# Optimization experiments

Hardware: AMD Instinct MI355X
Metric: run time of the kernel (lower is better)

Reference implementation:

```python
import jax, jax.numpy as jnp
import numpy as np

NUM_HEADS = 8
WIN = 3


def setup_inputs() -> dict:
    key = jax.random.key(0)
    ks = jax.random.split(key, 7)
    C = 64
    b, H, W = 8, 64, 64
    x = jax.random.normal(ks[0], (b, C, H, W), jnp.float32)
    W_qk = jax.random.normal(ks[1], (C, 2 * C), jnp.float32) * 0.05
    b_qk = jax.random.normal(ks[2], (2 * C,), jnp.float32) * 0.05
    W_kv = jax.random.normal(ks[3], (C, 2 * C), jnp.float32) * 0.05
    b_kv = jax.random.normal(ks[4], (2 * C,), jnp.float32) * 0.05
    W_proj = jax.random.normal(ks[5], (C, C), jnp.float32) * 0.05
    b_proj = jax.random.normal(ks[6], (C,), jnp.float32) * 0.05
    return {"x": x, "W_qk": W_qk, "b_qk": b_qk, "W_kv": W_kv, "b_kv": b_kv,
            "W_proj": W_proj, "b_proj": b_proj}


def reference(x, W_qk, b_qk, W_kv, b_kv, W_proj, b_proj):
    b, C, H, W = x.shape
    hd = C // NUM_HEADS
    scale = hd ** -0.5
    B = b * H * W
    L = WIN * WIN

    # Reflection pad (1,1,1,1) then extract all 3x3 windows (stride 1) -> one window per pixel.
    xp = jnp.pad(x, ((0, 0), (0, 0), (1, 1), (1, 1)), mode="reflect")  # (b,C,H+2,W+2)
    patches = jnp.stack(
        [xp[:, :, i:i + H, j:j + W] for i in range(WIN) for j in range(WIN)],
        axis=2,
    )  # (b, C, 9, H, W)
    patches = jnp.transpose(patches, (0, 3, 4, 1, 2))  # (b, H, W, C, 9)
    # Faithful to torch: contiguous (B, C, 3, 3).reshape(B, L, C) scrambles C and L.
    xs = patches.reshape(B, L, C)  # (B, 9, C) -- scrambled layout, as in original

    # pooling_size=1 -> AvgPool2d identity; g_pooling = mean over the 9 tokens
    x_g = jnp.mean(xs, axis=1, keepdims=True)            # (B, 1, C)
    x_f = jnp.concatenate([x_g, xs], axis=1)             # (B, 10, C)
    N = x_f.shape[1]

    # x_raw: per-pixel token, order (b h w) matches window order
    x_raw = jnp.transpose(x, (0, 2, 3, 1)).reshape(B, C)  # (B, C)

    # q / q_ projections
    qk = x_raw @ W_qk + b_qk                              # (B, 2C)
    q = qk[:, :C].reshape(B, NUM_HEADS, hd)               # (B, h, d)
    q_ = qk[:, C:].reshape(B, NUM_HEADS, hd)              # (B, h, d)
    q_value = jnp.sum(q * q_, axis=-1, keepdims=True)     # (B, h, 1)

    # k / v projections over pooled-global + window tokens
    kv = (x_f @ W_kv + b_kv).reshape(B, N, 2, NUM_HEADS, hd)
    k = jnp.transpose(kv[:, :, 0], (0, 2, 1, 3))          # (B, h, N, d)
    v = jnp.transpose(kv[:, :, 1], (0, 2, 1, 3))          # (B, h, N, d)

    logits = jnp.einsum("bhd,bhnd->bhn", q * scale, k)    # (B, h, N)
    logits = jnp.concatenate([logits, q_value], axis=-1)  # (B, h, N+1)
    attn = jax.nn.softmax(logits, axis=-1)

    x_fusion = jnp.einsum("bhn,bhnd->bhd", attn[..., :N], v)  # (B, h, d)
    x_sole = attn[..., N:] * q_                               # (B, h, d)
    out = (x_sole + x_fusion).reshape(B, C)                   # concat heads

    out = out @ W_proj + b_proj                               # (B, C)
    out = out.reshape(b, H, W, C).transpose(0, 3, 1, 2)       # (b, C, H, W)
    return out
```

## Files before the change

### kernel.cpp

```cpp
#include <hip/hip_runtime.h>
#include <math.h>
#include <stdint.h>


#define GS 432
#define RS 72
#define A0 3456
#define B0 5504
#define C0 6528
#define D0 7552

typedef _Float16 h2 __attribute__((ext_vector_type(2)));

static __device__ __forceinline__ h2 h2_of(uint32_t u) {
    return __builtin_bit_cast(h2, u);
}

__global__ __launch_bounds__(256, 2) void pix_attn_main(
    const float* __restrict__ x,
    const float* __restrict__ W_qk,
    const float* __restrict__ b_qk,
    const float* __restrict__ W_kv,
    const float* __restrict__ b_kv,
    const float* __restrict__ W_proj,
    const float* __restrict__ b_proj,
    float* __restrict__ out)
{
    __shared__ uint32_t smem[8576];

    const int tid = threadIdx.x;
    const int j    = blockIdx.x;
    const int g_   = j >> 4;
    const int tile = g_ * 8 + (j & 7);
    const int hg   = (j >> 3) & 1;
    const int bb   = tile >> 6;
    const int t_id = tile & 63;
    const int h0r  = (t_id >> 2) << 2;
    const int w0c  = (t_id & 3) << 4;

    const float* xb = x + (size_t)bb * (64 * 64 * 64);
#pragma unroll
    for (int it = 0; it < 14; ++it) {
        int idx = it * 256 + tid;
        if (idx < 3456) {
            int pair = idx / 108;
            int pix  = idx - pair * 108;
            int r    = pix / 18;
            int cc   = pix - r * 18;
            int gq   = pair >> 2;
            int w    = pair & 3;
            int gr   = h0r + r - 1;
            gr = (gr < 0) ? 1 : ((gr > 63) ? 62 : gr);
            int gc   = w0c + cc - 1;
            gc = (gc < 0) ? 1 : ((gc > 63) ? 62 : gc);
            const float* p0 = xb + ((pair * 2) << 12) + (gr << 6) + gc;
            h2 pk = { (_Float16)p0[0], (_Float16)p0[4096] };
            smem[gq * GS + r * RS + cc * 4 + w] = __builtin_bit_cast(uint32_t, pk);
        }
    }

    h2* wA = (h2*)(smem + A0);
    h2* wB = (h2*)(smem + B0);
    h2* wC = (h2*)(smem + C0);
    h2* wD = (h2*)(smem + D0);
#pragma unroll
    for (int it = 0; it < 8; ++it) {
        int idx = it * 256 + tid;
        int hh = idx >> 9, dd = (idx >> 5) & 15, p = idx & 31;
        int h  = hg * 4 + hh;
        int col = (dd < 8) ? (h * 8 + dd) : (64 + h * 8 + (dd & 7));
        wA[idx] = h2{ (_Float16)W_qk[(2 * p) * 128 + col],
                      (_Float16)W_qk[(2 * p + 1) * 128 + col] };
    }
#pragma unroll
    for (int it = 0; it < 4; ++it) {
        int idx = it * 256 + tid;
        int hh = idx >> 8, c = (idx >> 2) & 63, dp = idx & 3;
        int h  = hg * 4 + hh;
        wB[idx] = h2{ (_Float16)W_kv[c * 128 + h * 8 + 2 * dp],
                      (_Float16)W_kv[c * 128 + h * 8 + 2 * dp + 1] };
    }
#pragma unroll
    for (int it = 0; it < 4; ++it) {
        int idx = it * 256 + tid;
        int hh = idx >> 8, dd = (idx >> 5) & 7, p = idx & 31;
        int h  = hg * 4 + hh;
        int col = 64 + h * 8 + dd;
        wC[idx] = h2{ (_Float16)W_kv[(2 * p) * 128 + col],
                      (_Float16)W_kv[(2 * p + 1) * 128 + col] };
    }
#pragma unroll
    for (int it = 0; it < 4; ++it) {
        int idx = it * 256 + tid;
        int jj = idx >> 4, p = idx & 15;
        wD[idx] = h2{ (_Float16)W_proj[(hg * 32 + 2 * p) * 64 + jj],
                      (_Float16)W_proj[(hg * 32 + 2 * p + 1) * 64 + jj] };
    }
    __syncthreads();

    const int wv   = __builtin_amdgcn_readfirstlane(tid >> 6);
    const int h8   = (hg * 4 + wv) << 3;
    const int lane = tid & 63;
    const int tr   = lane >> 4;
    const int tc   = lane & 15;
    const uint32_t* xl4 = smem + tr * RS + tc * 4;
    const float scale = 0.35355339059327373f;

    float q[8], qp[8];
    {
        h2 a2[16];
        float acc16[16];
#pragma unroll
        for (int dd = 0; dd < 16; ++dd) acc16[dd] = 0.f;
#pragma unroll
        for (int half = 0; half < 2; ++half) {
#pragma unroll
            for (int g = 0; g < 4; ++g) {
                uint4 v = *(const uint4*)(xl4 + (half * 4 + g) * GS + RS + 4);
#pragma unroll
                for (int w = 0; w < 4; ++w)
                    a2[4 * g + w] = h2_of((&v.x)[w]);
            }
#pragma unroll
            for (int dd = 0; dd < 16; ++dd) {
                const uint4* wr4 =
                    (const uint4*)(wA + wv * 512 + dd * 32 + half * 16);
                float acc = acc16[dd];
#pragma unroll
                for (int p4 = 0; p4 < 4; ++p4) {
                    uint4 wv4 = wr4[p4];
#pragma unroll
                    for (int w = 0; w < 4; ++w)
                        acc = __builtin_amdgcn_fdot2(a2[p4 * 4 + w],
                                                     h2_of((&wv4.x)[w]),
                                                     acc, false);
                }
                acc16[dd] = acc;
            }
            __builtin_amdgcn_sched_barrier(0);
        }
#pragma unroll
        for (int dd = 0; dd < 16; ++dd) {
            if (dd < 8) q[dd] = b_qk[h8 + dd] + acc16[dd];
            else        qp[dd & 7] = b_qk[64 + h8 + (dd & 7)] + acc16[dd];
        }
    }
    float qv = 0.f, beta = 0.f;
#pragma unroll
    for (int d = 0; d < 8; ++d) {
        qv   = fmaf(q[d], qp[d], qv);
        beta = fmaf(q[d], b_kv[h8 + d], beta);
    }
    h2 q2[4];
#pragma unroll
    for (int dp = 0; dp < 4; ++dp)
        q2[dp] = h2{ (_Float16)q[2 * dp], (_Float16)q[2 * dp + 1] };
    __builtin_amdgcn_sched_barrier(0);

    h2 u2[64];
    float uf0[9];
#pragma unroll
    for (int c = 0; c < 64; ++c) {
        uint4 wv4 = *(const uint4*)(wB + wv * 256 + c * 4);
        float s = 0.f;
#pragma unroll
        for (int dp = 0; dp < 4; ++dp)
            s = __builtin_amdgcn_fdot2(q2[dp], h2_of((&wv4.x)[dp]), s, false);
        u2[c].x = (_Float16)s;
        if (c < 9) uf0[c] = s;
        else       u2[c - 9].y = (_Float16)s;
        if ((c & 31) == 31) __builtin_amdgcn_sched_barrier(0);
    }
#pragma unroll
    for (int c = 55; c < 64; ++c)
        u2[c].y = (_Float16)uf0[c + 9 - 64];

    float lg[9];
#pragma unroll
    for (int t = 0; t < 9; ++t) lg[t] = 0.f;
#pragma unroll
    for (int g = 0; g < 8; ++g) {
#pragma unroll
        for (int l = 0; l < 9; ++l) {
            const int wi = l / 3;
            const int wj = l - wi * 3;
            uint4 v = *(const uint4*)(xl4 + g * GS + wi * RS + wj * 4);
#pragma unroll
            for (int w = 0; w < 4; ++w) {
                h2 hv = h2_of((&v.x)[w]);
                const int f0 = 9 * (8 * g + 2 * w) + l;
                const int c0 = f0 & 63;
                const int t0 = f0 >> 6;
                if (c0 < 55) {
                    lg[t0] = __builtin_amdgcn_fdot2(hv, u2[c0], lg[t0], false);
                } else {
                    lg[t0]     = fmaf((float)hv.x, (float)u2[c0].x, lg[t0]);
                    lg[t0 + 1] = fmaf((float)hv.y, (float)u2[c0].y, lg[t0 + 1]);
                }
            }
        }
        if ((g & 3) == 3) __builtin_amdgcn_sched_barrier(0);
    }

    float pn[9], Pn = 0.f, pqv;
    {
        float lgs = 0.f, l2[11];
#pragma unroll
        for (int t = 0; t < 9; ++t) {
            lgs += lg[t];
            l2[t] = (lg[t] + beta) * scale;
        }
        l2[9]  = (lgs * (1.f / 9.f) + beta) * scale;
        l2[10] = qv;
        float m = l2[0];
#pragma unroll
        for (int i = 1; i < 11; ++i) m = fmaxf(m, l2[i]);
        float pp[11], den = 0.f;
#pragma unroll
        for (int i = 0; i < 11; ++i) { pp[i] = __expf(l2[i] - m); den += pp[i]; }
        float inv = 1.f / den;
#pragma unroll
        for (int t = 0; t < 9; ++t) {
            pn[t] = (pp[t] + pp[9] * (1.f / 9.f)) * inv;
            Pn += pn[t];
        }
        pqv = pp[10] * inv;
    }
    h2 pn2[9], pn2b[8];
#pragma unroll
    for (int t = 0; t < 9; ++t) pn2[t] = h2{ (_Float16)pn[t], (_Float16)pn[t] };
#pragma unroll
    for (int t = 0; t < 8; ++t) pn2b[t] = h2{ (_Float16)pn[t], (_Float16)pn[t + 1] };

    h2 y2[64];
#pragma unroll
    for (int c = 0; c < 64; ++c) y2[c] = h2{ (_Float16)0.f, (_Float16)0.f };
#pragma unroll
    for (int g = 0; g < 8; ++g) {
#pragma unroll
        for (int l = 0; l < 9; ++l) {
            const int wi = l / 3;
            const int wj = l - wi * 3;
            uint4 v = *(const uint4*)(xl4 + g * GS + wi * RS + wj * 4);
#pragma unroll
            for (int w = 0; w < 4; ++w) {
                h2 a = h2_of((&v.x)[w]);
                const int f0 = 9 * (8 * g + 2 * w) + l;
                const int c0 = f0 & 63;
                const int t0 = f0 >> 6;
                h2 m2 = (c0 < 55) ? pn2[t0] : pn2b[t0];
                y2[c0] = y2[c0] + m2 * a;
            }
        }
        if ((g & 3) == 3) __builtin_amdgcn_sched_barrier(0);
    }

    h2 y2c[32];
#pragma unroll
    for (int p = 0; p < 32; ++p) {
        float ylo = (float)y2[2 * p].x     + (float)y2[(2 * p + 55) & 63].y;
        float yhi = (float)y2[2 * p + 1].x + (float)y2[(2 * p + 56) & 63].y;
        y2c[p] = h2{ (_Float16)ylo, (_Float16)yhi };
    }
    __builtin_amdgcn_sched_barrier(0);

    float o[8];
#pragma unroll
    for (int dd = 0; dd < 8; ++dd) {
        const uint4* wr4 = (const uint4*)(wC + wv * 256 + dd * 32);
        float acc = fmaf(pqv, qp[dd], Pn * b_kv[64 + h8 + dd]);
#pragma unroll
        for (int p4 = 0; p4 < 8; ++p4) {
            uint4 wv4 = wr4[p4];
#pragma unroll
            for (int w = 0; w < 4; ++w)
                acc = __builtin_amdgcn_fdot2(y2c[p4 * 4 + w],
                                             h2_of((&wv4.x)[w]), acc, false);
        }
        o[dd] = acc;
    }
    __builtin_amdgcn_sched_barrier(0);

    __syncthreads();
    float* pre = (float*)smem;
#pragma unroll
    for (int d = 0; d < 8; ++d)
        pre[lane * 33 + (wv << 3) + d] = o[d];
    __syncthreads();

    const int j0 = wv << 4;
    const float* pl = pre + lane * 33;
    h2 pre2[16];
#pragma unroll
    for (int p = 0; p < 16; ++p)
        pre2[p] = h2{ (_Float16)pl[2 * p], (_Float16)pl[2 * p + 1] };
    float o2[16];
#pragma unroll
    for (int jj = 0; jj < 16; ++jj) {
        const uint4* wr4 = (const uint4*)(wD + (j0 + jj) * 16);
        float acc = (hg == 0) ? b_proj[j0 + jj] : 0.f;
#pragma unroll
        for (int p4 = 0; p4 < 4; ++p4) {
            uint4 wv4 = wr4[p4];
#pragma unroll
            for (int w = 0; w < 4; ++w)
                acc = __builtin_amdgcn_fdot2(pre2[p4 * 4 + w],
                                             h2_of((&wv4.x)[w]), acc, false);
        }
        o2[jj] = acc;
    }
    float* ob = out + (size_t)bb * (64 * 64 * 64);
    const int pr = h0r + tr, pc = w0c + tc;
#pragma unroll
    for (int jj = 0; jj < 16; ++jj)
        unsafeAtomicAdd(&ob[((j0 + jj) << 12) + (pr << 6) + pc], o2[jj]);
}

extern "C" void kernel_launch(void* const* d_in, const int* in_sizes, int n_in,
                              void* d_out, int out_size, void* d_ws, size_t ws_size,
                              hipStream_t stream)
{
    const float* x      = (const float*)d_in[0];
    const float* W_qk   = (const float*)d_in[1];
    const float* b_qk   = (const float*)d_in[2];
    const float* W_kv   = (const float*)d_in[3];
    const float* b_kv   = (const float*)d_in[4];
    const float* W_proj = (const float*)d_in[5];
    const float* b_proj = (const float*)d_in[6];
    float* out = (float*)d_out;

    hipMemsetAsync(out, 0, (size_t)out_size * sizeof(float), stream);
    pix_attn_main<<<1024, 256, 0, stream>>>(x, W_qk, b_qk, W_kv, b_kv,
                                            W_proj, b_proj, out);
}
```

Measured before the change: 60.85 us.

## Process all heads per block in two passes, drop atomics and memset

Each block now handles one spatial tile for all eight heads by looping over two head passes, instead of splitting heads across two blocks. This avoids loading and converting the input tile twice and removes the output memset and the atomic accumulation, replacing them with plain stores after a full-width projection. The trade-off is half as many blocks, a serial dependency between passes, and more shared memory per block, which can lower occupancy.

```diff
diff --git a/kernel.cpp b/kernel.cpp
--- a/kernel.cpp
+++ b/kernel.cpp
@@ -6,9 +6,9 @@
 #define GS 432
 #define RS 72
 #define A0 3456
-#define B0 5504
-#define C0 6528
-#define D0 7552
+#define B0 7552
+#define C0 9600
+#define D0 11648
 
 typedef _Float16 h2 __attribute__((ext_vector_type(2)));
 
@@ -26,13 +26,10 @@
     const float* __restrict__ b_proj,
     float* __restrict__ out)
 {
-    __shared__ uint32_t smem[8576];
-
-    const int tid = threadIdx.x;
-    const int j    = blockIdx.x;
-    const int g_   = j >> 4;
-    const int tile = g_ * 8 + (j & 7);
-    const int hg   = (j >> 3) & 1;
+    __shared__ uint32_t smem[13696];
+
+    const int tid  = threadIdx.x;
+    const int tile = blockIdx.x;
     const int bb   = tile >> 6;
     const int t_id = tile & 63;
     const int h0r  = (t_id >> 2) << 2;
@@ -64,243 +61,250 @@
     h2* wC = (h2*)(smem + C0);
     h2* wD = (h2*)(smem + D0);
 #pragma unroll
-    for (int it = 0; it < 8; ++it) {
-        int idx = it * 256 + tid;
-        int hh = idx >> 9, dd = (idx >> 5) & 15, p = idx & 31;
-        int h  = hg * 4 + hh;
+    for (int it = 0; it < 16; ++it) {
+        int idx = it * 256 + tid;
+        int h = idx >> 9, dd = (idx >> 5) & 15, p = idx & 31;
         int col = (dd < 8) ? (h * 8 + dd) : (64 + h * 8 + (dd & 7));
         wA[idx] = h2{ (_Float16)W_qk[(2 * p) * 128 + col],
                       (_Float16)W_qk[(2 * p + 1) * 128 + col] };
     }
 #pragma unroll
-    for (int it = 0; it < 4; ++it) {
-        int idx = it * 256 + tid;
-        int hh = idx >> 8, c = (idx >> 2) & 63, dp = idx & 3;
-        int h  = hg * 4 + hh;
+    for (int it = 0; it < 8; ++it) {
+        int idx = it * 256 + tid;
+        int h = idx >> 8, c = (idx >> 2) & 63, dp = idx & 3;
         wB[idx] = h2{ (_Float16)W_kv[c * 128 + h * 8 + 2 * dp],
                       (_Float16)W_kv[c * 128 + h * 8 + 2 * dp + 1] };
     }
 #pragma unroll
-    for (int it = 0; it < 4; ++it) {
-        int idx = it * 256 + tid;
-        int hh = idx >> 8, dd = (idx >> 5) & 7, p = idx & 31;
-        int h  = hg * 4 + hh;
+    for (int it = 0; it < 8; ++it) {
+        int idx = it * 256 + tid;
+        int h = idx >> 8, dd = (idx >> 5) & 7, p = idx & 31;
         int col = 64 + h * 8 + dd;
         wC[idx] = h2{ (_Float16)W_kv[(2 * p) * 128 + col],
                       (_Float16)W_kv[(2 * p + 1) * 128 + col] };
     }
 #pragma unroll
-    for (int it = 0; it < 4; ++it) {
-        int idx = it * 256 + tid;
-        int jj = idx >> 4, p = idx & 15;
-        wD[idx] = h2{ (_Float16)W_proj[(hg * 32 + 2 * p) * 64 + jj],
-                      (_Float16)W_proj[(hg * 32 + 2 * p + 1) * 64 + jj] };
+    for (int it = 0; it < 8; ++it) {
+        int idx = it * 256 + tid;
+        int jj = idx >> 5, p = idx & 31;
+        wD[idx] = h2{ (_Float16)W_proj[(2 * p) * 64 + jj],
+                      (_Float16)W_proj[(2 * p + 1) * 64 + jj] };
     }
     __syncthreads();
 
     const int wv   = __builtin_amdgcn_readfirstlane(tid >> 6);
-    const int h8   = (hg * 4 + wv) << 3;
     const int lane = tid & 63;
     const int tr   = lane >> 4;
     const int tc   = lane & 15;
     const uint32_t* xl4 = smem + tr * RS + tc * 4;
     const float scale = 0.35355339059327373f;
 
-    float q[8], qp[8];
+#pragma unroll 1
+    for (int pass = 0; pass < 2; ++pass) {
+        const int head = pass * 4 + wv;
+        const int h8   = head << 3;
+
+        float q[8], qp[8];
+        {
+            h2 a2[16];
+            float acc16[16];
+#pragma unroll
+            for (int dd = 0; dd < 16; ++dd) acc16[dd] = 0.f;
+#pragma unroll
+            for (int half = 0; half < 2; ++half) {
+#pragma unroll
+                for (int g = 0; g < 4; ++g) {
+                    uint4 v = *(const uint4*)(xl4 + (half * 4 + g) * GS + RS + 4);
+#pragma unroll
+                    for (int w = 0; w < 4; ++w)
+                        a2[4 * g + w] = h2_of((&v.x)[w]);
+                }
+#pragma unroll
+                for (int dd = 0; dd < 16; ++dd) {
+                    const uint4* wr4 =
+                        (const uint4*)(wA + head * 512 + dd * 32 + half * 16);
+                    float acc = acc16[dd];
+#pragma unroll
+                    for (int p4 = 0; p4 < 4; ++p4) {
+                        uint4 wv4 = wr4[p4];
+#pragma unroll
+                        for (int w = 0; w < 4; ++w)
+                            acc = __builtin_amdgcn_fdot2(a2[p4 * 4 + w],
+                                                         h2_of((&wv4.x)[w]),
+                                                         acc, false);
+                    }
+                    acc16[dd] = acc;
+                }
+                __builtin_amdgcn_sched_barrier(0);
+            }
+#pragma unroll
+            for (int dd = 0; dd < 16; ++dd) {
+                if (dd < 8) q[dd] = b_qk[h8 + dd] + acc16[dd];
+                else        qp[dd & 7] = b_qk[64 + h8 + (dd & 7)] + acc16[dd];
+            }
+        }
+        float qv = 0.f, beta = 0.f;
+#pragma unroll
+        for (int d = 0; d < 8; ++d) {
+            qv   = fmaf(q[d], qp[d], qv);
+            beta = fmaf(q[d], b_kv[h8 + d], beta);
+        }
+        h2 q2[4];
+#pragma unroll
+        for (int dp = 0; dp < 4; ++dp)
+            q2[dp] = h2{ (_Float16)q[2 * dp], (_Float16)q[2 * dp + 1] };
+        __builtin_amdgcn_sched_barrier(0);
+
+        h2 u2[64];
+        float uf0[9];
+#pragma unroll
+        for (int c = 0; c < 64; ++c) {
+            uint4 wv4 = *(const uint4*)(wB + head * 256 + c * 4);
+            float s = 0.f;
+#pragma unroll
+            for (int dp = 0; dp < 4; ++dp)
+                s = __builtin_amdgcn_fdot2(q2[dp], h2_of((&wv4.x)[dp]), s, false);
+            u2[c].x = (_Float16)s;
+            if (c < 9) uf0[c] = s;
+            else       u2[c - 9].y = (_Float16)s;
+            if ((c & 31) == 31) __builtin_amdgcn_sched_barrier(0);
+        }
+#pragma unroll
+        for (int c = 55; c < 64; ++c)
+            u2[c].y = (_Float16)uf0[c + 9 - 64];
+
+        float lg[9];
+#pragma unroll
+        for (int t = 0; t < 9; ++t) lg[t] = 0.f;
+#pragma unroll
+        for (int g = 0; g < 8; ++g) {
+#pragma unroll
+            for (int l = 0; l < 9; ++l) {
+                const int wi = l / 3;
+                const int wj = l - wi * 3;
+                uint4 v = *(const uint4*)(xl4 + g * GS + wi * RS + wj * 4);
+#pragma unroll
+                for (int w = 0; w < 4; ++w) {
+                    h2 hv = h2_of((&v.x)[w]);
+                    const int f0 = 9 * (8 * g + 2 * w) + l;
+                    const int c0 = f0 & 63;
+                    const int t0 = f0 >> 6;
+                    if (c0 < 55) {
+                        lg[t0] = __builtin_amdgcn_fdot2(hv, u2[c0], lg[t0], false);
+                    } else {
+                        lg[t0]     = fmaf((float)hv.x, (float)u2[c0].x, lg[t0]);
+                        lg[t0 + 1] = fmaf((float)hv.y, (float)u2[c0].y, lg[t0 + 1]);
+                    }
+                }
+            }
+            if ((g & 3) == 3) __builtin_amdgcn_sched_barrier(0);
+        }
+
+        float pn[9], Pn = 0.f, pqv;
+        {
+            float lgs = 0.f, l2[11];
+#pragma unroll
+            for (int t = 0; t < 9; ++t) {
+                lgs += lg[t];
+                l2[t] = (lg[t] + beta) * scale;
+            }
+            l2[9]  = (lgs * (1.f / 9.f) + beta) * scale;
+            l2[10] = qv;
+            float m = l2[0];
+#pragma unroll
+            for (int i = 1; i < 11; ++i) m = fmaxf(m, l2[i]);
+            float pp[11], den = 0.f;
+#pragma unroll
+            for (int i = 0; i < 11; ++i) { pp[i] = __expf(l2[i] - m); den += pp[i]; }
+            float inv = 1.f / den;
+#pragma unroll
+            for (int t = 0; t < 9; ++t) {
+                pn[t] = (pp[t] + pp[9] * (1.f / 9.f)) * inv;
+                Pn += pn[t];
+            }
+            pqv = pp[10] * inv;
+        }
+        h2 pn2[9], pn2b[8];
+#pragma unroll
+        for (int t = 0; t < 9; ++t) pn2[t] = h2{ (_Float16)pn[t], (_Float16)pn[t] };
+#pragma unroll
+        for (int t = 0; t < 8; ++t) pn2b[t] = h2{ (_Float16)pn[t], (_Float16)pn[t + 1] };
+
+        h2 y2[64];
+#pragma unroll
+        for (int c = 0; c < 64; ++c) y2[c] = h2{ (_Float16)0.f, (_Float16)0.f };
+#pragma unroll
+        for (int g = 0; g < 8; ++g) {
+#pragma unroll
+            for (int l = 0; l < 9; ++l) {
+                const int wi = l / 3;
+                const int wj = l - wi * 3;
+                uint4 v = *(const uint4*)(xl4 + g * GS + wi * RS + wj * 4);
+#pragma unroll
+                for (int w = 0; w < 4; ++w) {
+                    h2 a = h2_of((&v.x)[w]);
+                    const int f0 = 9 * (8 * g + 2 * w) + l;
+                    const int c0 = f0 & 63;
+                    const int t0 = f0 >> 6;
+                    h2 m2 = (c0 < 55) ? pn2[t0] : pn2b[t0];
+                    y2[c0] = y2[c0] + m2 * a;
+                }
+            }
+            if ((g & 3) == 3) __builtin_amdgcn_sched_barrier(0);
+        }
+
+        h2 y2c[32];
+#pragma unroll
+        for (int p = 0; p < 32; ++p) {
+            float ylo = (float)y2[2 * p].x     + (float)y2[(2 * p + 55) & 63].y;
+            float yhi = (float)y2[2 * p + 1].x + (float)y2[(2 * p + 56) & 63].y;
+            y2c[p] = h2{ (_Float16)ylo, (_Float16)yhi };
+        }
+        __builtin_amdgcn_sched_barrier(0);
+
+        float o[8];
+#pragma unroll
+        for (int dd = 0; dd < 8; ++dd) {
+            const uint4* wr4 = (const uint4*)(wC + head * 256 + dd * 32);
+            float acc = fmaf(pqv, qp[dd], Pn * b_kv[64 + h8 + dd]);
+#pragma unroll
+            for (int p4 = 0; p4 < 8; ++p4) {
+                uint4 wv4 = wr4[p4];
+#pragma unroll
+                for (int w = 0; w < 4; ++w)
+                    acc = __builtin_amdgcn_fdot2(y2c[p4 * 4 + w],
+                                                 h2_of((&wv4.x)[w]), acc, false);
+            }
+            o[dd] = acc;
+        }
+
+        __syncthreads();
+        uint32_t* st = smem + A0 + pass * 2048 + lane * 17 + (wv << 2);
+#pragma unroll
+        for (int k = 0; k < 4; ++k)
+            st[k] = __builtin_bit_cast(uint32_t,
+                        h2{ (_Float16)o[2 * k], (_Float16)o[2 * k + 1] });
+    }
+    __syncthreads();
+
+    const int j0 = wv << 4;
+    h2 pre2[32];
     {
-        h2 a2[16];
-        float acc16[16];
-#pragma unroll
-        for (int dd = 0; dd < 16; ++dd) acc16[dd] = 0.f;
-#pragma unroll
-        for (int half = 0; half < 2; ++half) {
-#pragma unroll
-            for (int g = 0; g < 4; ++g) {
-                uint4 v = *(const uint4*)(xl4 + (half * 4 + g) * GS + RS + 4);
-#pragma unroll
-                for (int w = 0; w < 4; ++w)
-                    a2[4 * g + w] = h2_of((&v.x)[w]);
-            }
-#pragma unroll
-            for (int dd = 0; dd < 16; ++dd) {
-                const uint4* wr4 =
-                    (const uint4*)(wA + wv * 512 + dd * 32 + half * 16);
-                float acc = acc16[dd];
-#pragma unroll
-                for (int p4 = 0; p4 < 4; ++p4) {
-                    uint4 wv4 = wr4[p4];
-#pragma unroll
-                    for (int w = 0; w < 4; ++w)
-                        acc = __builtin_amdgcn_fdot2(a2[p4 * 4 + w],
-                                                     h2_of((&wv4.x)[w]),
-                                                     acc, false);
-                }
-                acc16[dd] = acc;
-            }
-            __builtin_amdgcn_sched_barrier(0);
-        }
-#pragma unroll
-        for (int dd = 0; dd < 16; ++dd) {
-            if (dd < 8) q[dd] = b_qk[h8 + dd] + acc16[dd];
-            else        qp[dd & 7] = b_qk[64 + h8 + (dd & 7)] + acc16[dd];
-        }
-    }
-    float qv = 0.f, beta = 0.f;
-#pragma unroll
-    for (int d = 0; d < 8; ++d) {
-        qv   = fmaf(q[d], qp[d], qv);
-        beta = fmaf(q[d], b_kv[h8 + d], beta);
-    }
-    h2 q2[4];
-#pragma unroll
-    for (int dp = 0; dp < 4; ++dp)
-        q2[dp] = h2{ (_Float16)q[2 * dp], (_Float16)q[2 * dp + 1] };
-    __builtin_amdgcn_sched_barrier(0);
-
-    h2 u2[64];
-    float uf0[9];
-#pragma unroll
-    for (int c = 0; c < 64; ++c) {
-        uint4 wv4 = *(const uint4*)(wB + wv * 256 + c * 4);
-        float s = 0.f;
-#pragma unroll
-        for (int dp = 0; dp < 4; ++dp)
-            s = __builtin_amdgcn_fdot2(q2[dp], h2_of((&wv4.x)[dp]), s, false);
-        u2[c].x = (_Float16)s;
-        if (c < 9) uf0[c] = s;
-        else       u2[c - 9].y = (_Float16)s;
-        if ((c & 31) == 31) __builtin_amdgcn_sched_barrier(0);
-    }
-#pragma unroll
-    for (int c = 55; c < 64; ++c)
-        u2[c].y = (_Float16)uf0[c + 9 - 64];
-
-    float lg[9];
-#pragma unroll
-    for (int t = 0; t < 9; ++t) lg[t] = 0.f;
-#pragma unroll
-    for (int g = 0; g < 8; ++g) {
-#pragma unroll
-        for (int l = 0; l < 9; ++l) {
-            const int wi = l / 3;
-            const int wj = l - wi * 3;
-            uint4 v = *(const uint4*)(xl4 + g * GS + wi * RS + wj * 4);
-#pragma unroll
-            for (int w = 0; w < 4; ++w) {
-                h2 hv = h2_of((&v.x)[w]);
-                const int f0 = 9 * (8 * g + 2 * w) + l;
-                const int c0 = f0 & 63;
-                const int t0 = f0 >> 6;
-                if (c0 < 55) {
-                    lg[t0] = __builtin_amdgcn_fdot2(hv, u2[c0], lg[t0], false);
-                } else {
-                    lg[t0]     = fmaf((float)hv.x, (float)u2[c0].x, lg[t0]);
-                    lg[t0 + 1] = fmaf((float)hv.y, (float)u2[c0].y, lg[t0 + 1]);
-                }
-            }
-        }
-        if ((g & 3) == 3) __builtin_amdgcn_sched_barrier(0);
-    }
-
-    float pn[9], Pn = 0.f, pqv;
-    {
-        float lgs = 0.f, l2[11];
-#pragma unroll
-        for (int t = 0; t < 9; ++t) {
-            lgs += lg[t];
-            l2[t] = (lg[t] + beta) * scale;
-        }
-        l2[9]  = (lgs * (1.f / 9.f) + beta) * scale;
-        l2[10] = qv;
-        float m = l2[0];
-#pragma unroll
-        for (int i = 1; i < 11; ++i) m = fmaxf(m, l2[i]);
-        float pp[11], den = 0.f;
-#pragma unroll
-        for (int i = 0; i < 11; ++i) { pp[i] = __expf(l2[i] - m); den += pp[i]; }
-        float inv = 1.f / den;
-#pragma unroll
-        for (int t = 0; t < 9; ++t) {
-            pn[t] = (pp[t] + pp[9] * (1.f / 9.f)) * inv;
-            Pn += pn[t];
-        }
-        pqv = pp[10] * inv;
-    }
-    h2 pn2[9], pn2b[8];
-#pragma unroll
-    for (int t = 0; t < 9; ++t) pn2[t] = h2{ (_Float16)pn[t], (_Float16)pn[t] };
-#pragma unroll
-    for (int t = 0; t < 8; ++t) pn2b[t] = h2{ (_Float16)pn[t], (_Float16)pn[t + 1] };
-
-    h2 y2[64];
-#pragma unroll
-    for (int c = 0; c < 64; ++c) y2[c] = h2{ (_Float16)0.f, (_Float16)0.f };
-#pragma unroll
-    for (int g = 0; g < 8; ++g) {
-#pragma unroll
-        for (int l = 0; l < 9; ++l) {
-            const int wi = l / 3;
-            const int wj = l - wi * 3;
-            uint4 v = *(const uint4*)(xl4 + g * GS + wi * RS + wj * 4);
-#pragma unroll
-            for (int w = 0; w < 4; ++w) {
-                h2 a = h2_of((&v.x)[w]);
-                const int f0 = 9 * (8 * g + 2 * w) + l;
-                const int c0 = f0 & 63;
-                const int t0 = f0 >> 6;
-                h2 m2 = (c0 < 55) ? pn2[t0] : pn2b[t0];
-                y2[c0] = y2[c0] + m2 * a;
-            }
-        }
-        if ((g & 3) == 3) __builtin_amdgcn_sched_barrier(0);
-    }
-
-    h2 y2c[32];
-#pragma unroll
-    for (int p = 0; p < 32; ++p) {
-        float ylo = (float)y2[2 * p].x     + (float)y2[(2 * p + 55) & 63].y;
-        float yhi = (float)y2[2 * p + 1].x + (float)y2[(2 * p + 56) & 63].y;
-        y2c[p] = h2{ (_Float16)ylo, (_Float16)yhi };
-    }
-    __builtin_amdgcn_sched_barrier(0);
-
-    float o[8];
-#pragma unroll
-    for (int dd = 0; dd < 8; ++dd) {
-        const uint4* wr4 = (const uint4*)(wC + wv * 256 + dd * 32);
-        float acc = fmaf(pqv, qp[dd], Pn * b_kv[64 + h8 + dd]);
+        const uint32_t* s1 = smem + A0 + lane * 17;
+        const uint32_t* s2 = smem + A0 + 2048 + lane * 17;
+#pragma unroll
+        for (int p = 0; p < 16; ++p) {
+            pre2[p]      = h2_of(s1[p]);
+            pre2[16 + p] = h2_of(s2[p]);
+        }
+    }
+    float o2[16];
+#pragma unroll
+    for (int jj = 0; jj < 16; ++jj) {
+        const uint4* wr4 = (const uint4*)(wD + (j0 + jj) * 32);
+        float acc = b_proj[j0 + jj];
 #pragma unroll
         for (int p4 = 0; p4 < 8; ++p4) {
-            uint4 wv4 = wr4[p4];
-#pragma unroll
-            for (int w = 0; w < 4; ++w)
-                acc = __builtin_amdgcn_fdot2(y2c[p4 * 4 + w],
-                                             h2_of((&wv4.x)[w]), acc, false);
-        }
-        o[dd] = acc;
-    }
-    __builtin_amdgcn_sched_barrier(0);
-
-    __syncthreads();
-    float* pre = (float*)smem;
-#pragma unroll
-    for (int d = 0; d < 8; ++d)
-        pre[lane * 33 + (wv << 3) + d] = o[d];
-    __syncthreads();
-
-    const int j0 = wv << 4;
-    const float* pl = pre + lane * 33;
-    h2 pre2[16];
-#pragma unroll
-    for (int p = 0; p < 16; ++p)
-        pre2[p] = h2{ (_Float16)pl[2 * p], (_Float16)pl[2 * p + 1] };
-    float o2[16];
-#pragma unroll
-    for (int jj = 0; jj < 16; ++jj) {
-        const uint4* wr4 = (const uint4*)(wD + (j0 + jj) * 16);
-        float acc = (hg == 0) ? b_proj[j0 + jj] : 0.f;
-#pragma unroll
-        for (int p4 = 0; p4 < 4; ++p4) {
             uint4 wv4 = wr4[p4];
 #pragma unroll
             for (int w = 0; w < 4; ++w)
@@ -308,12 +312,13 @@
                                              h2_of((&wv4.x)[w]), acc, false);
         }
         o2[jj] = acc;
+        if ((jj & 3) == 3) __builtin_amdgcn_sched_barrier(0);
     }
     float* ob = out + (size_t)bb * (64 * 64 * 64);
     const int pr = h0r + tr, pc = w0c + tc;
 #pragma unroll
     for (int jj = 0; jj < 16; ++jj)
-        unsafeAtomicAdd(&ob[((j0 + jj) << 12) + (pr << 6) + pc], o2[jj]);
+        ob[((j0 + jj) << 12) + (pr << 6) + pc] = o2[jj];
 }
 
 extern "C" void kernel_launch(void* const* d_in, const int* in_sizes, int n_in,
@@ -329,7 +334,6 @@
     const float* b_proj = (const float*)d_in[6];
     float* out = (float*)d_out;
 
-    hipMemsetAsync(out, 0, (size_t)out_size * sizeof(float), stream);
-    pix_attn_main<<<1024, 256, 0, stream>>>(x, W_qk, b_qk, W_kv, b_kv,
-                                            W_proj, b_proj, out);
+    pix_attn_main<<<512, 256, 0, stream>>>(x, W_qk, b_qk, W_kv, b_kv,
+                                           W_proj, b_proj, out);
 }
```

New measurement: 87.41 us. +43.7%, slower.
